# Optimization experiments

Hardware: AMD Instinct MI355X
Metric: run time of the kernel (lower is better)

## Reference

```python
import jax, jax.numpy as jnp
import numpy as np

N = 50000; E = 150000
NODE_IN = 16; EDGE_IN = 19; H = 32  # H = max(2*node_in, 32)
LEAK = 0.1; EPS = 1e-5
LAYER_DINS = (16, 32, 32)


def _leaky(x):
    return jnp.where(x >= 0, x, LEAK * x)


def _bn(x, g, b):
    # BatchNorm1d in training mode: batch statistics, biased variance
    m = x.mean(0)
    v = x.var(0)
    return (x - m) * jax.lax.rsqrt(v + EPS) * g + b


def setup_inputs() -> dict:
    key = jax.random.key(0)
    keys = iter(jax.random.split(key, 64))

    def rn(shape, s=0.05):
        return jax.random.normal(next(keys), shape, dtype=jnp.float32) * s

    inp = {
        'x': jax.random.normal(next(keys), (N, NODE_IN), dtype=jnp.float32),
        'edge_index': jax.random.randint(next(keys), (2, E), 0, N),
        'e': jax.random.normal(next(keys), (E, EDGE_IN), dtype=jnp.float32),
        'xbatch': jnp.zeros((N,), dtype=jnp.int32),
        'bn_node_g': jnp.ones((NODE_IN,), jnp.float32), 'bn_node_b': jnp.zeros((NODE_IN,), jnp.float32),
        'bn_edge_g': jnp.ones((EDGE_IN,), jnp.float32), 'bn_edge_b': jnp.zeros((EDGE_IN,), jnp.float32),
    }
    for l, din in enumerate(LAYER_DINS):
        inp[f'l{l}_nnW1'] = rn((EDGE_IN, din));      inp[f'l{l}_nnb1'] = jnp.zeros((din,), jnp.float32)
        inp[f'l{l}_nnW2'] = rn((din, din * H));       inp[f'l{l}_nnb2'] = jnp.zeros((din * H,), jnp.float32)
        inp[f'l{l}_root'] = rn((din, H));             inp[f'l{l}_bias'] = jnp.zeros((H,), jnp.float32)
    # MetaLayer predictor: EdgeModel(H, EDGE_IN, leak) and NodeModel(H, 2, leak)
    inp['em_W1'] = rn((2 * H + EDGE_IN, H)); inp['em_b1'] = jnp.zeros((H,), jnp.float32)
    inp['em_W2'] = rn((H, H));               inp['em_b2'] = jnp.zeros((H,), jnp.float32)
    inp['nm1_W1'] = rn((2 * H, H));          inp['nm1_b1'] = jnp.zeros((H,), jnp.float32)
    inp['nm1_W2'] = rn((H, H));              inp['nm1_b2'] = jnp.zeros((H,), jnp.float32)
    inp['nm2_W1'] = rn((2 * H, H));          inp['nm2_b1'] = jnp.zeros((H,), jnp.float32)
    inp['nm2_W2'] = rn((H, 2));              inp['nm2_b2'] = jnp.zeros((2,), jnp.float32)
    return inp


def _forward(x, e, edge_index, p):
    (bn_node_g, bn_node_b, bn_edge_g, bn_edge_b,
     l0_nnW1, l0_nnb1, l0_nnW2, l0_nnb2, l0_root, l0_bias,
     l1_nnW1, l1_nnb1, l1_nnW2, l1_nnb2, l1_root, l1_bias,
     l2_nnW1, l2_nnb1, l2_nnW2, l2_nnb2, l2_root, l2_bias,
     em_W1, em_b1, em_W2, em_b2,
     nm1_W1, nm1_b1, nm1_W2, nm1_b2,
     nm2_W1, nm2_b1, nm2_W2, nm2_b2) = p

    e = _bn(e, bn_edge_g, bn_edge_b)
    x = _bn(x, bn_node_g, bn_node_b)
    row, col = edge_index[0], edge_index[1]  # source, target (PyG convention)

    layers = [(l0_nnW1, l0_nnb1, l0_nnW2, l0_nnb2, l0_root, l0_bias),
              (l1_nnW1, l1_nnb1, l1_nnW2, l1_nnb2, l1_root, l1_bias),
              (l2_nnW1, l2_nnb1, l2_nnW2, l2_nnb2, l2_root, l2_bias)]
    for (W1, b1, W2, b2, root, bias), din in zip(layers, LAYER_DINS):
        # edge MLP -> per-edge weight matrix [E, din, H]
        w = _leaky(_leaky(e @ W1 + b1) @ W2 + b2).reshape(E, din, H)
        msg = jnp.einsum('ei,eio->eo', x[row], w)              # gather + per-edge matvec
        agg = jax.ops.segment_sum(msg, col, num_segments=N)     # scatter-add ('add' aggr)
        x = agg + x @ root + bias                                # NNConv root weight + bias

    # MetaLayer predictor
    e2 = _leaky(jnp.concatenate([x[row], x[col], e], axis=1) @ em_W1 + em_b1) @ em_W2 + em_b2
    h = _leaky(jnp.concatenate([x[row], e2], axis=1) @ nm1_W1 + nm1_b1) @ nm1_W2 + nm1_b2
    cnt = jnp.clip(jax.ops.segment_sum(jnp.ones((E,), x.dtype), col, num_segments=N), 1.0)
    agg = jax.ops.segment_sum(h, col, num_segments=N) / cnt[:, None]
    xo = _leaky(jnp.concatenate([x, agg], axis=1) @ nm2_W1 + nm2_b1) @ nm2_W2 + nm2_b2
    return jax.nn.log_softmax(xo, axis=1)  # [N, 2] node_pred


def reference(x, edge_index, e, xbatch,
              bn_node_g, bn_node_b, bn_edge_g, bn_edge_b,
              l0_nnW1, l0_nnb1, l0_nnW2, l0_nnb2, l0_root, l0_bias,
              l1_nnW1, l1_nnb1, l1_nnW2, l1_nnb2, l1_root, l1_bias,
              l2_nnW1, l2_nnb1, l2_nnW2, l2_nnb2, l2_root, l2_bias,
              em_W1, em_b1, em_W2, em_b2,
              nm1_W1, nm1_b1, nm1_W2, nm1_b2,
              nm2_W1, nm2_b1, nm2_W2, nm2_b2):
    p = (bn_node_g, bn_node_b, bn_edge_g, bn_edge_b,
         l0_nnW1, l0_nnb1, l0_nnW2, l0_nnb2, l0_root, l0_bias,
         l1_nnW1, l1_nnb1, l1_nnW2, l1_nnb2, l1_root, l1_bias,
         l2_nnW1, l2_nnb1, l2_nnW2, l2_nnb2, l2_root, l2_bias,
         em_W1, em_b1, em_W2, em_b2,
         nm1_W1, nm1_b1, nm1_W2, nm1_b2,
         nm2_W1, nm2_b1, nm2_W2, nm2_b2)
    return _forward(x, e, edge_index, p)
```

## Files before the change

### kernel.cpp

```cpp
#include <hip/hip_runtime.h>
#include <math.h>

constexpr int NN  = 50000;
constexpr int NE  = 150000;
constexpr int NIN = 16;
constexpr int EIN = 19;
constexpr int HD  = 32;
constexpr int NTILES = NE / 16;
constexpr int NBLK_E = 128;
constexpr int NBLK_X = 64;

#define LEAK  0.1f
#define BNEPS 1e-5f

typedef __attribute__((ext_vector_type(8))) short bfrag;
typedef __attribute__((ext_vector_type(4))) float f32x4;
typedef __attribute__((ext_vector_type(2))) float f32x2;
typedef __attribute__((ext_vector_type(4))) int   i32x4;

__device__ __forceinline__ float lky(float v){ return fmaxf(v, LEAK*v); }
__device__ __forceinline__ unsigned f2bf(float f){
  unsigned u = __float_as_uint(f);
  return ((u + 0x7FFFu + ((u >> 16) & 1u)) >> 16);
}
__device__ __forceinline__ void split8(const float* v, i32x4& h4, i32x4& l4){
  unsigned hs[8], ls[8];
  #pragma unroll
  for(int j = 0; j < 8; j++){
    unsigned hh = f2bf(v[j]);
    float hf = __uint_as_float(hh << 16);
    hs[j] = hh; ls[j] = f2bf(v[j] - hf);
  }
  h4[0] = (int)(hs[0] | (hs[1]<<16)); h4[1] = (int)(hs[2] | (hs[3]<<16));
  h4[2] = (int)(hs[4] | (hs[5]<<16)); h4[3] = (int)(hs[6] | (hs[7]<<16));
  l4[0] = (int)(ls[0] | (ls[1]<<16)); l4[1] = (int)(ls[2] | (ls[3]<<16));
  l4[2] = (int)(ls[4] | (ls[5]<<16)); l4[3] = (int)(ls[6] | (ls[7]<<16));
}

__global__ void zero_kernel(float* __restrict__ p, int n){
  int stride = gridDim.x * blockDim.x;
  for(int i = blockIdx.x*blockDim.x + threadIdx.x; i < n; i += stride) p[i] = 0.f;
}

__global__ __launch_bounds__(256) void stats_all_kernel(const float* __restrict__ e,
                                                        const float* __restrict__ x,
                                                        float* __restrict__ partial_e,
                                                        float* __restrict__ partial_x){
  __shared__ float red[4][40];
  const int tid = threadIdx.x, lane = tid & 63, wid = tid >> 6;
  if(blockIdx.x < NBLK_E){
    float s[EIN], q[EIN];
    #pragma unroll
    for(int c = 0; c < EIN; c++){ s[c] = 0.f; q[c] = 0.f; }
    const int gstride = NBLK_E * 256;
    for(int g = blockIdx.x*256 + tid; g < NE/4; g += gstride){
      const f32x4* p = (const f32x4*)(e + (size_t)g * 76);
      #pragma unroll
      for(int m = 0; m < 19; m++){
        f32x4 v = p[m];
        #pragma unroll
        for(int j = 0; j < 4; j++){
          int c = (4*m + j) % 19;
          s[c] += v[j]; q[c] = fmaf(v[j], v[j], q[c]);
        }
      }
    }
    #pragma unroll
    for(int off = 32; off; off >>= 1){
      #pragma unroll
      for(int c = 0; c < EIN; c++){ s[c] += __shfl_xor(s[c], off); q[c] += __shfl_xor(q[c], off); }
    }
    if(lane == 0){
      #pragma unroll
      for(int c = 0; c < EIN; c++){ red[wid][c] = s[c]; red[wid][20 + c] = q[c]; }
    }
    __syncthreads();
    if(tid < 39 && tid != 19)
      partial_e[blockIdx.x*40 + tid] = red[0][tid] + red[1][tid] + red[2][tid] + red[3][tid];
  } else {
    float s[NIN], q[NIN];
    #pragma unroll
    for(int c = 0; c < NIN; c++){ s[c] = 0.f; q[c] = 0.f; }
    const int bid = blockIdx.x - NBLK_E;
    const int gstride = NBLK_X * 256;
    for(int r = bid*256 + tid; r < NN; r += gstride){
      const f32x4* p = (const f32x4*)(x + (size_t)r * NIN);
      #pragma unroll
      for(int m = 0; m < 4; m++){
        f32x4 v = p[m];
        #pragma unroll
        for(int j = 0; j < 4; j++){
          int c = 4*m + j;
          s[c] += v[j]; q[c] = fmaf(v[j], v[j], q[c]);
        }
      }
    }
    #pragma unroll
    for(int off = 32; off; off >>= 1){
      #pragma unroll
      for(int c = 0; c < NIN; c++){ s[c] += __shfl_xor(s[c], off); q[c] += __shfl_xor(q[c], off); }
    }
    if(lane == 0){
      #pragma unroll
      for(int c = 0; c < NIN; c++){ red[wid][c] = s[c]; red[wid][16 + c] = q[c]; }
    }
    __syncthreads();
    if(tid < 32)
      partial_x[bid*32 + tid] = red[0][tid] + red[1][tid] + red[2][tid] + red[3][tid];
  }
}

__global__ __launch_bounds__(1024) void prep_kernel(const float* __restrict__ partial_e,
                                                    const float* __restrict__ partial_x,
                                                    const float* __restrict__ ge, const float* __restrict__ be,
                                                    const float* __restrict__ gx, const float* __restrict__ bx,
                                                    const float* __restrict__ l0W1, const float* __restrict__ l0b1,
                                                    const float* __restrict__ l1W1, const float* __restrict__ l1b1,
                                                    const float* __restrict__ l2W1, const float* __restrict__ l2b1,
                                                    const float* __restrict__ emW1, const float* __restrict__ emb1,
                                                    const float* __restrict__ emW2, const float* __restrict__ emb2,
                                                    const float* __restrict__ nm1W1, const float* __restrict__ nm1b1,
                                                    const float* __restrict__ nm1W2, const float* __restrict__ nm1b2,
                                                    float* __restrict__ ss_g, float* __restrict__ W1f,
                                                    float* __restrict__ b1f, float* __restrict__ biasP,
                                                    short* __restrict__ predpk){
  __shared__ float ss[70];
  __shared__ float emW1f[608];
  __shared__ float emb1f[32];
  __shared__ float predW[7168];
  const int t = threadIdx.x;

  if(t < EIN){
    float s = 0.f, q = 0.f;
    for(int b = 0; b < NBLK_E; b++){ s += partial_e[b*40 + t]; q += partial_e[b*40 + 20 + t]; }
    float m = s / (float)NE;
    float v = q / (float)NE - m*m;
    float sc = ge[t] * rsqrtf(v + BNEPS);
    ss[t] = sc; ss[EIN + t] = be[t] - m*sc;
  } else if(t >= 32 && t < 32 + NIN){
    int c = t - 32;
    float s = 0.f, q = 0.f;
    for(int b = 0; b < NBLK_X; b++){ s += partial_x[b*32 + c]; q += partial_x[b*32 + 16 + c]; }
    float m = s / (float)NN;
    float v = q / (float)NN - m*m;
    float sc = gx[c] * rsqrtf(v + BNEPS);
    ss[2*EIN + c] = sc; ss[2*EIN + NIN + c] = bx[c] - m*sc;
  }
  __syncthreads();
  if(t < 70) ss_g[t] = ss[t];

  if(t < 128){
    int seg = t >> 5, j = t & 31;
    if(seg == 0){
      if(j < NIN){
        float acc = l0b1[j];
        for(int k = 0; k < EIN; k++){
          W1f[0*640 + k*NIN + j] = ss[k] * l0W1[k*NIN + j];
          acc += ss[EIN+k] * l0W1[k*NIN + j];
        }
        b1f[0*32 + j] = acc;
      }
    } else if(seg == 1){
      float acc = l1b1[j];
      for(int k = 0; k < EIN; k++){
        W1f[1*640 + k*HD + j] = ss[k] * l1W1[k*HD + j];
        acc += ss[EIN+k] * l1W1[k*HD + j];
      }
      b1f[1*32 + j] = acc;
    } else if(seg == 2){
      float acc = l2b1[j];
      for(int k = 0; k < EIN; k++){
        W1f[2*640 + k*HD + j] = ss[k] * l2W1[k*HD + j];
        acc += ss[EIN+k] * l2W1[k*HD + j];
      }
      b1f[2*32 + j] = acc;
    } else {
      float acc = emb1[j];
      for(int k = 0; k < EIN; k++){
        emW1f[k*HD + j] = ss[k] * emW1[(2*HD+k)*HD + j];
        acc += ss[EIN+k] * emW1[(2*HD+k)*HD + j];
      }
      emb1f[j] = acc;
    }
  }
  __syncthreads();

  for(int i = t; i < 224*32; i += 1024){
    int k = i >> 5, n = i & 31;
    float v;
    if(k < 64)       v = emW1[k*32 + n];
    else if(k < 83)  v = emW1f[(k-64)*32 + n];
    else if(k < 96)  v = 0.f;
    else if(k < 128) v = emW2[(k-96)*32 + n];
    else if(k < 192) v = nm1W1[(k-128)*32 + n];
    else             v = nm1W2[(k-192)*32 + n];
    predW[i] = v;
  }
  if(t < 128){
    int s = t >> 5, n = t & 31;
    biasP[t] = (s==0) ? emb1f[n] : (s==1) ? emb2[n] : (s==2) ? nm1b1[n] : nm1b2[n];
  }
  __syncthreads();

  for(int idx = t; idx < 14*512; idx += 1024){
    int c = idx >> 9, l = (idx >> 3) & 63, j = idx & 7;
    int kbg = c >> 1, nc = c & 1;
    int k = kbg*32 + 8*(l>>4) + j;
    int n = nc*16 + (l & 15);
    predpk[idx] = (short)f2bf(predW[k*32 + n]);
  }
}

__global__ __launch_bounds__(256) void w2pack_all_kernel(const float* __restrict__ W20,
                                                         const float* __restrict__ W21,
                                                         const float* __restrict__ W22,
                                                         short* __restrict__ w2pk){
  int idx = blockIdx.x*256 + threadIdx.x;
  if(idx >= 81920) return;
  const float* W2; int DIN, base, ci;
  if(idx < 16384){ W2 = W20; DIN = 16; base = 0;     ci = idx; }
  else if(idx < 49152){ W2 = W21; DIN = 32; base = 32768; ci = idx - 16384; }
  else { W2 = W22; DIN = 32; base = 65536; ci = idx - 49152; }
  int c = ci >> 9, l = (ci >> 3) & 63, j = ci & 7;
  int k = 8*(l>>4) + j;
  int n = c*16 + (l & 15);
  float v = (k < DIN) ? W2[(size_t)k*(DIN*HD) + n] : 0.f;
  w2pk[base + ci] = (short)f2bf(v);
}

__global__ __launch_bounds__(256) void norm_root_kernel(const float* __restrict__ x,
                                                        const float* __restrict__ ssx,
                                                        const float* __restrict__ root,
                                                        const float* __restrict__ bias,
                                                        float* __restrict__ x_bn,
                                                        float* __restrict__ x_a){
  __shared__ float rs[NIN*HD];
  __shared__ float scs[NIN], shs[NIN], bs[HD];
  const int tid = threadIdx.x;
  for(int i = tid; i < NIN*HD; i += 256) rs[i] = root[i];
  if(tid < NIN){ scs[tid] = ssx[tid]; shs[tid] = ssx[NIN + tid]; }
  else if(tid < NIN + HD) bs[tid - NIN] = bias[tid - NIN];
  __syncthreads();

  int n = blockIdx.x*256 + tid;
  if(n >= NN) return;
  float xb[NIN];
  const f32x4* xp = (const f32x4*)(x + (size_t)n*NIN);
  #pragma unroll
  for(int g = 0; g < 4; g++){
    f32x4 v = xp[g];
    #pragma unroll
    for(int j = 0; j < 4; j++) xb[g*4+j] = fmaf(v[j], scs[g*4+j], shs[g*4+j]);
  }
  f32x4* obn = (f32x4*)(x_bn + (size_t)n*NIN);
  #pragma unroll
  for(int g = 0; g < 4; g++){
    f32x4 v; v[0]=xb[g*4]; v[1]=xb[g*4+1]; v[2]=xb[g*4+2]; v[3]=xb[g*4+3];
    obn[g] = v;
  }
  f32x4 a0 = *(const f32x4*)&bs[0],  a1 = *(const f32x4*)&bs[4];
  f32x4 a2 = *(const f32x4*)&bs[8],  a3 = *(const f32x4*)&bs[12];
  f32x4 a4 = *(const f32x4*)&bs[16], a5 = *(const f32x4*)&bs[20];
  f32x4 a6 = *(const f32x4*)&bs[24], a7 = *(const f32x4*)&bs[28];
  #pragma unroll
  for(int k = 0; k < NIN; k++){
    float v = xb[k];
    const f32x4* wp = (const f32x4*)&rs[k*HD];
    a0 = __builtin_elementwise_fma((f32x4){v,v,v,v}, wp[0], a0);
    a1 = __builtin_elementwise_fma((f32x4){v,v,v,v}, wp[1], a1);
    a2 = __builtin_elementwise_fma((f32x4){v,v,v,v}, wp[2], a2);
    a3 = __builtin_elementwise_fma((f32x4){v,v,v,v}, wp[3], a3);
    a4 = __builtin_elementwise_fma((f32x4){v,v,v,v}, wp[4], a4);
    a5 = __builtin_elementwise_fma((f32x4){v,v,v,v}, wp[5], a5);
    a6 = __builtin_elementwise_fma((f32x4){v,v,v,v}, wp[6], a6);
    a7 = __builtin_elementwise_fma((f32x4){v,v,v,v}, wp[7], a7);
  }
  f32x4* outp = (f32x4*)(x_a + (size_t)n*HD);
  outp[0]=a0; outp[1]=a1; outp[2]=a2; outp[3]=a3;
  outp[4]=a4; outp[5]=a5; outp[6]=a6; outp[7]=a7;
}

__global__ __launch_bounds__(256) void t1all_kernel(const float* __restrict__ eraw,
                                                    const float* __restrict__ W1f,
                                                    const float* __restrict__ b1f,
                                                    short* __restrict__ T10,
                                                    short* __restrict__ T11,
                                                    short* __restrict__ T12){
  int e = blockIdx.x*256 + threadIdx.x;
  if(e >= NE) return;
  const float* ep = eraw + (size_t)e*EIN;
  float eb[EIN];
  #pragma unroll
  for(int k = 0; k < EIN; k++) eb[k] = ep[k];

  {
    float tv[16];
    #pragma unroll
    for(int j = 0; j < 16; j++) tv[j] = b1f[j];
    #pragma unroll
    for(int k = 0; k < EIN; k++){
      float v = eb[k];
      #pragma unroll
      for(int j = 0; j < 16; j++) tv[j] = fmaf(v, W1f[k*16 + j], tv[j]);
    }
    unsigned pk[8];
    #pragma unroll
    for(int p = 0; p < 8; p++){
      float a = tv[2*p], b = tv[2*p+1];
      pk[p] = f2bf(fmaxf(a, LEAK*a)) | (f2bf(fmaxf(b, LEAK*b)) << 16);
    }
    i32x4* outp = (i32x4*)(T10 + (size_t)e*32);
    i32x4 v0; v0[0]=(int)pk[0]; v0[1]=(int)pk[1]; v0[2]=(int)pk[2]; v0[3]=(int)pk[3];
    i32x4 v1; v1[0]=(int)pk[4]; v1[1]=(int)pk[5]; v1[2]=(int)pk[6]; v1[3]=(int)pk[7];
    i32x4 zz; zz[0]=0; zz[1]=0; zz[2]=0; zz[3]=0;
    outp[0] = v0; outp[1] = v1; outp[2] = zz; outp[3] = zz;
  }
  #pragma unroll
  for(int l = 1; l < 3; l++){
    const float* Wl = W1f + l*640;
    const float* bl = b1f + l*32;
    short* Tl = (l == 1) ? T11 : T12;
    float tv[32];
    #pragma unroll
    for(int j = 0; j < 32; j++) tv[j] = bl[j];
    #pragma unroll
    for(int k = 0; k < EIN; k++){
      float v = eb[k];
      #pragma unroll
      for(int j = 0; j < 32; j++) tv[j] = fmaf(v, Wl[k*32 + j], tv[j]);
    }
    unsigned pk[16];
    #pragma unroll
    for(int p = 0; p < 16; p++){
      float a = tv[2*p], b = tv[2*p+1];
      pk[p] = f2bf(fmaxf(a, LEAK*a)) | (f2bf(fmaxf(b, LEAK*b)) << 16);
    }
    i32x4* outp = (i32x4*)(Tl + (size_t)e*32);
    #pragma unroll
    for(int g = 0; g < 4; g++){
      i32x4 v; v[0]=(int)pk[g*4]; v[1]=(int)pk[g*4+1]; v[2]=(int)pk[g*4+2]; v[3]=(int)pk[g*4+3];
      outp[g] = v;
    }
  }
}

template<int DIN>
__global__ __launch_bounds__(256) void rootv2_kernel(const float* __restrict__ xin,
                                                     const float* __restrict__ root,
                                                     const float* __restrict__ bias,
                                                     float* __restrict__ xout){
  int n = blockIdx.x*256 + threadIdx.x;
  if(n >= NN) return;
  float xr[DIN];
  const f32x4* xp = (const f32x4*)(xin + (size_t)n*DIN);
  #pragma unroll
  for(int g = 0; g < DIN/4; g++){ f32x4 v = xp[g];
    #pragma unroll
    for(int j = 0; j < 4; j++) xr[g*4+j] = v[j]; }
  float acc[HD];
  #pragma unroll
  for(int o = 0; o < HD; o++) acc[o] = bias[o];
  #pragma unroll
  for(int k = 0; k < DIN; k++){
    float v = xr[k];
    #pragma unroll
    for(int o = 0; o < HD; o++) acc[o] = fmaf(v, root[k*HD + o], acc[o]);
  }
  f32x4* outp = (f32x4*)(xout + (size_t)n*HD);
  #pragma unroll
  for(int g = 0; g < 8; g++){ f32x4 v; v[0]=acc[g*4]; v[1]=acc[g*4+1]; v[2]=acc[g*4+2]; v[3]=acc[g*4+3]; outp[g] = v; }
}

template<int DIN, int NCH, int HALVES>
__global__ __launch_bounds__(512) void msg6_kernel(const short* __restrict__ T1,
                                                   const int* __restrict__ rowp,
                                                   const int* __restrict__ colp,
                                                   const float* __restrict__ xin,
                                                   const short* __restrict__ w2p,
                                                   const float* __restrict__ b2,
                                                   float* __restrict__ xout){
  constexpr int CH = NCH / HALVES;
  __shared__ short w2s[CH*512];
  __shared__ float b2s[NCH*16];
  __shared__ float xgs[8][DIN][16];

  const int tid = threadIdx.x;
  const int l   = tid & 63;
  const int wid = tid >> 6;
  const int grp = l >> 4, lo16 = l & 15;
  const int tile = blockIdx.x*8 + wid;
  const bool active = tile < NTILES;
  const int e0 = tile * 16;

  if(active){
    int r = rowp[e0 + lo16];
    if(DIN == 32){
      const f32x4* xp = (const f32x4*)(xin + (size_t)r*32 + grp*8);
      f32x4 a = xp[0], b = xp[1];
      #pragma unroll
      for(int j = 0; j < 4; j++) xgs[wid][grp*8 + j][lo16]     = a[j];
      #pragma unroll
      for(int j = 0; j < 4; j++) xgs[wid][grp*8 + 4 + j][lo16] = b[j];
    } else {
      const f32x4* xp = (const f32x4*)(xin + (size_t)r*16 + grp*4);
      f32x4 a = xp[0];
      #pragma unroll
      for(int j = 0; j < 4; j++) xgs[wid][grp*4 + j][lo16] = a[j];
    }
  }

  bfrag af = {0,0,0,0,0,0,0,0};
  if(active) af = *(const bfrag*)(T1 + (size_t)(e0 + lo16)*32 + grp*8);

  f32x2 m0a = {0.f,0.f}, m0b = {0.f,0.f}, m1a = {0.f,0.f}, m1b = {0.f,0.f};

  for(int h = 0; h < HALVES; h++){
    if(h) __syncthreads();
    for(int t = tid; t < CH*64; t += 512)
      ((i32x4*)w2s)[t] = ((const i32x4*)w2p)[h*CH*64 + t];
    if(h == 0)
      for(int t = tid; t < NCH*16; t += 512) b2s[t] = b2[t];
    __syncthreads();

    if(active){
      #pragma unroll 4
      for(int i = 0; i < CH/2; i++){
        const int cg = h*CH + 2*i;
        const int ig = cg >> 1;
        float bv0 = b2s[cg*16 + lo16];
        float bv1 = b2s[(cg+1)*16 + lo16];
        f32x4 c0 = {bv0,bv0,bv0,bv0};
        f32x4 c1 = {bv1,bv1,bv1,bv1};
        bfrag b0 = *(const bfrag*)&w2s[((2*i  )*64 + l)*8];
        bfrag b1 = *(const bfrag*)&w2s[((2*i+1)*64 + l)*8];
        f32x4 u0 = __builtin_amdgcn_mfma_f32_16x16x32_bf16(af, b0, c0, 0, 0, 0);
        f32x4 u1 = __builtin_amdgcn_mfma_f32_16x16x32_bf16(af, b1, c1, 0, 0, 0);

        f32x4 xv = *(const f32x4*)&xgs[wid][ig][grp*4];
        f32x2 xva = {xv[0], xv[1]}, xvb = {xv[2], xv[3]};
        f32x2 u0a = {u0[0],u0[1]}, u0b = {u0[2],u0[3]};
        f32x2 u1a = {u1[0],u1[1]}, u1b = {u1[2],u1[3]};
        f32x2 a0a = __builtin_elementwise_max(u0a, u0a*LEAK);
        f32x2 a0b = __builtin_elementwise_max(u0b, u0b*LEAK);
        f32x2 a1a = __builtin_elementwise_max(u1a, u1a*LEAK);
        f32x2 a1b = __builtin_elementwise_max(u1b, u1b*LEAK);
        m0a = __builtin_elementwise_fma(xva, a0a, m0a);
        m0b = __builtin_elementwise_fma(xvb, a0b, m0b);
        m1a = __builtin_elementwise_fma(xva, a1a, m1a);
        m1b = __builtin_elementwise_fma(xvb, a1b, m1b);
      }
    }
  }

  if(active){
    float m0[4] = {m0a[0], m0a[1], m0b[0], m0b[1]};
    float m1[4] = {m1a[0], m1a[1], m1b[0], m1b[1]};
    #pragma unroll
    for(int reg = 0; reg < 4; reg++){
      int ce = colp[e0 + grp*4 + reg];
      atomicAdd(&xout[(size_t)ce*HD + lo16],      m0[reg]);
      atomicAdd(&xout[(size_t)ce*HD + 16 + lo16], m1[reg]);
    }
  }
}

__global__ __launch_bounds__(256, 4) void pred5_kernel(const float* __restrict__ x,
                                                       const float* __restrict__ eraw,
                                                       const int* __restrict__ rowp,
                                                       const int* __restrict__ colp,
                                                       const short* __restrict__ predpk,
                                                       const float* __restrict__ biasP,
                                                       float* __restrict__ agg,
                                                       float* __restrict__ cnt){
  __shared__ short fAhi[4][16][104];
  __shared__ short fAlo[4][16][104];
  __shared__ short uAhi[4][16][40];
  __shared__ short uAlo[4][16][40];

  const int tid = threadIdx.x;
  const int l = tid & 63, wid = tid >> 6;
  const int grp = l >> 4, lo16 = l & 15;

  bfrag wb[14];
  #pragma unroll
  for(int c = 0; c < 14; c++) wb[c] = *(const bfrag*)(predpk + ((size_t)c*64 + l)*8);
  float bP[8];
  #pragma unroll
  for(int s = 0; s < 4; s++){
    bP[s*2]   = biasP[s*32 + lo16];
    bP[s*2+1] = biasP[s*32 + 16 + lo16];
  }

  f32x4 z; z[0]=0.f; z[1]=0.f; z[2]=0.f; z[3]=0.f;
  const int tbase = (blockIdx.x*4 + wid) * 4;

  for(int tt = 0; tt < 4; tt++){
    const int tile = tbase + tt;
    if(tile >= NTILES) break;
    const int e0 = tile * 16;

    {
      float v[8];
      i32x4 h4, l4;
      int r = rowp[e0 + lo16];
      const float* xp = x + (size_t)r*32 + grp*8;
      #pragma unroll
      for(int j = 0; j < 8; j++) v[j] = xp[j];
      split8(v, h4, l4);
      *(i32x4*)&fAhi[wid][lo16][grp*8] = h4;
      *(i32x4*)&fAlo[wid][lo16][grp*8] = l4;

      int c = colp[e0 + lo16];
      const float* xq = x + (size_t)c*32 + grp*8;
      #pragma unroll
      for(int j = 0; j < 8; j++) v[j] = xq[j];
      split8(v, h4, l4);
      *(i32x4*)&fAhi[wid][lo16][32 + grp*8] = h4;
      *(i32x4*)&fAlo[wid][lo16][32 + grp*8] = l4;

      const float* ep = eraw + (size_t)(e0 + lo16)*EIN;
      #pragma unroll
      for(int j = 0; j < 8; j++){ int f = grp*8 + j; v[j] = (f < EIN) ? ep[f] : 0.f; }
      split8(v, h4, l4);
      *(i32x4*)&fAhi[wid][lo16][64 + grp*8] = h4;
      *(i32x4*)&fAlo[wid][lo16][64 + grp*8] = l4;
    }

    #pragma unroll
    for(int nc = 0; nc < 2; nc++){
      f32x4 acc = z;
      #pragma unroll
      for(int kb = 0; kb < 3; kb++){
        bfrag ah = *(const bfrag*)&fAhi[wid][lo16][kb*32 + grp*8];
        bfrag al = *(const bfrag*)&fAlo[wid][lo16][kb*32 + grp*8];
        acc = __builtin_amdgcn_mfma_f32_16x16x32_bf16(ah, wb[kb*2 + nc], acc, 0, 0, 0);
        acc = __builtin_amdgcn_mfma_f32_16x16x32_bf16(al, wb[kb*2 + nc], acc, 0, 0, 0);
      }
      int n = nc*16 + lo16;
      float bv = bP[nc];
      #pragma unroll
      for(int reg = 0; reg < 4; reg++){
        float uv = acc[reg] + bv; uv = fmaxf(uv, LEAK*uv);
        unsigned hh = f2bf(uv);
        float hf = __uint_as_float(hh << 16);
        uAhi[wid][grp*4 + reg][n] = (short)hh;
        uAlo[wid][grp*4 + reg][n] = (short)f2bf(uv - hf);
      }
    }

    #pragma unroll
    for(int nc = 0; nc < 2; nc++){
      f32x4 acc = z;
      bfrag ah = *(const bfrag*)&uAhi[wid][lo16][grp*8];
      bfrag al = *(const bfrag*)&uAlo[wid][lo16][grp*8];
      acc = __builtin_amdgcn_mfma_f32_16x16x32_bf16(ah, wb[6 + nc], acc, 0, 0, 0);
      acc = __builtin_amdgcn_mfma_f32_16x16x32_bf16(al, wb[6 + nc], acc, 0, 0, 0);
      int n = nc*16 + lo16;
      float bv = bP[2 + nc];
      #pragma unroll
      for(int reg = 0; reg < 4; reg++){
        float ev = acc[reg] + bv;
        unsigned hh = f2bf(ev);
        float hf = __uint_as_float(hh << 16);
        fAhi[wid][grp*4 + reg][32 + n] = (short)hh;
        fAlo[wid][grp*4 + reg][32 + n] = (short)f2bf(ev - hf);
      }
    }

    #pragma unroll
    for(int nc = 0; nc < 2; nc++){
      f32x4 acc = z;
      #pragma unroll
      for(int kb = 0; kb < 2; kb++){
        bfrag ah = *(const bfrag*)&fAhi[wid][lo16][kb*32 + grp*8];
        bfrag al = *(const bfrag*)&fAlo[wid][lo16][kb*32 + grp*8];
        acc = __builtin_amdgcn_mfma_f32_16x16x32_bf16(ah, wb[8 + kb*2 + nc], acc, 0, 0, 0);
        acc = __builtin_amdgcn_mfma_f32_16x16x32_bf16(al, wb[8 + kb*2 + nc], acc, 0, 0, 0);
      }
      int n = nc*16 + lo16;
      float bv = bP[4 + nc];
      #pragma unroll
      for(int reg = 0; reg < 4; reg++){
        float vv = acc[reg] + bv; vv = fmaxf(vv, LEAK*vv);
        unsigned hh = f2bf(vv);
        float hf = __uint_as_float(hh << 16);
        uAhi[wid][grp*4 + reg][n] = (short)hh;
        uAlo[wid][grp*4 + reg][n] = (short)f2bf(vv - hf);
      }
    }

    int ce[4];
    #pragma unroll
    for(int reg = 0; reg < 4; reg++) ce[reg] = colp[e0 + grp*4 + reg];

    #pragma unroll
    for(int nc = 0; nc < 2; nc++){
      f32x4 acc = z;
      bfrag ah = *(const bfrag*)&uAhi[wid][lo16][grp*8];
      bfrag al = *(const bfrag*)&uAlo[wid][lo16][grp*8];
      acc = __builtin_amdgcn_mfma_f32_16x16x32_bf16(ah, wb[12 + nc], acc, 0, 0, 0);
      acc = __builtin_amdgcn_mfma_f32_16x16x32_bf16(al, wb[12 + nc], acc, 0, 0, 0);
      int n = nc*16 + lo16;
      float bv = bP[6 + nc];
      #pragma unroll
      for(int reg = 0; reg < 4; reg++)
        atomicAdd(&agg[(size_t)ce[reg]*HD + n], acc[reg] + bv);
    }

    if(l < 16) atomicAdd(&cnt[colp[e0 + l]], 1.f);
  }
}

__global__ __launch_bounds__(256) void final2_kernel(const float* __restrict__ x,
                                                     const float* __restrict__ agg,
                                                     const float* __restrict__ cnt,
                                                     const float* __restrict__ W1,
                                                     const float* __restrict__ b1,
                                                     const float* __restrict__ W2,
                                                     const float* __restrict__ b2,
                                                     float* __restrict__ out){
  __shared__ float w1s[2*HD*HD];
  __shared__ float w2s[HD*2];
  __shared__ float b1s[HD];
  __shared__ float b2s[2];
  const int tid = threadIdx.x;
  for(int i = tid; i < 2*HD*HD; i += 256) w1s[i] = W1[i];
  if(tid < 64) w2s[tid] = W2[tid];
  if(tid < HD) b1s[tid] = b1[tid];
  if(tid < 2)  b2s[tid] = b2[tid];
  __syncthreads();

  int n = blockIdx.x*256 + tid;
  if(n >= NN) return;
  float inv = 1.f / fmaxf(cnt[n], 1.f);

  float xin[HD], ain[HD];
  const f32x4* xp = (const f32x4*)(x + (size_t)n*HD);
  const f32x4* ap = (const f32x4*)(agg + (size_t)n*HD);
  #pragma unroll
  for(int g = 0; g < 8; g++){
    f32x4 v = xp[g];
    #pragma unroll
    for(int j = 0; j < 4; j++) xin[g*4+j] = v[j];
  }
  #pragma unroll
  for(int g = 0; g < 8; g++){
    f32x4 v = ap[g];
    #pragma unroll
    for(int j = 0; j < 4; j++) ain[g*4+j] = v[j] * inv;
  }

  f32x4 a0 = *(const f32x4*)&b1s[0],  a1 = *(const f32x4*)&b1s[4];
  f32x4 a2 = *(const f32x4*)&b1s[8],  a3 = *(const f32x4*)&b1s[12];
  f32x4 a4 = *(const f32x4*)&b1s[16], a5 = *(const f32x4*)&b1s[20];
  f32x4 a6 = *(const f32x4*)&b1s[24], a7 = *(const f32x4*)&b1s[28];
  #pragma unroll
  for(int k = 0; k < HD; k++){
    float v = xin[k];
    const f32x4* wp = (const f32x4*)&w1s[k*HD];
    f32x4 vv = {v,v,v,v};
    a0 = __builtin_elementwise_fma(vv, wp[0], a0);
    a1 = __builtin_elementwise_fma(vv, wp[1], a1);
    a2 = __builtin_elementwise_fma(vv, wp[2], a2);
    a3 = __builtin_elementwise_fma(vv, wp[3], a3);
    a4 = __builtin_elementwise_fma(vv, wp[4], a4);
    a5 = __builtin_elementwise_fma(vv, wp[5], a5);
    a6 = __builtin_elementwise_fma(vv, wp[6], a6);
    a7 = __builtin_elementwise_fma(vv, wp[7], a7);
  }
  #pragma unroll
  for(int k = 0; k < HD; k++){
    float v = ain[k];
    const f32x4* wp = (const f32x4*)&w1s[(HD+k)*HD];
    f32x4 vv = {v,v,v,v};
    a0 = __builtin_elementwise_fma(vv, wp[0], a0);
    a1 = __builtin_elementwise_fma(vv, wp[1], a1);
    a2 = __builtin_elementwise_fma(vv, wp[2], a2);
    a3 = __builtin_elementwise_fma(vv, wp[3], a3);
    a4 = __builtin_elementwise_fma(vv, wp[4], a4);
    a5 = __builtin_elementwise_fma(vv, wp[5], a5);
    a6 = __builtin_elementwise_fma(vv, wp[6], a6);
    a7 = __builtin_elementwise_fma(vv, wp[7], a7);
  }

  float t[HD];
  *(f32x4*)&t[0]  = a0; *(f32x4*)&t[4]  = a1; *(f32x4*)&t[8]  = a2; *(f32x4*)&t[12] = a3;
  *(f32x4*)&t[16] = a4; *(f32x4*)&t[20] = a5; *(f32x4*)&t[24] = a6; *(f32x4*)&t[28] = a7;

  float o0 = b2s[0], o1 = b2s[1];
  #pragma unroll
  for(int k = 0; k < HD; k++){
    float v = lky(t[k]);
    o0 = fmaf(v, w2s[k*2],   o0);
    o1 = fmaf(v, w2s[k*2+1], o1);
  }

  float m  = fmaxf(o0, o1);
  float ls = m + logf(expf(o0 - m) + expf(o1 - m));
  out[(size_t)n*2]   = o0 - ls;
  out[(size_t)n*2+1] = o1 - ls;
}

extern "C" void kernel_launch(void* const* d_in, const int* in_sizes, int n_in,
                              void* d_out, int out_size, void* d_ws, size_t ws_size,
                              hipStream_t stream){
  const float* x  = (const float*)d_in[0];
  const int*   ei = (const int*)  d_in[1];
  const float* e  = (const float*)d_in[2];
  const float* bn_node_g = (const float*)d_in[4];
  const float* bn_node_b = (const float*)d_in[5];
  const float* bn_edge_g = (const float*)d_in[6];
  const float* bn_edge_b = (const float*)d_in[7];
  const float* lW1[3], *lb1[3], *lW2[3], *lb2[3], *lroot[3], *lbias[3];
  for(int l = 0; l < 3; l++){
    lW1[l]   = (const float*)d_in[8 + 6*l + 0];
    lb1[l]   = (const float*)d_in[8 + 6*l + 1];
    lW2[l]   = (const float*)d_in[8 + 6*l + 2];
    lb2[l]   = (const float*)d_in[8 + 6*l + 3];
    lroot[l] = (const float*)d_in[8 + 6*l + 4];
    lbias[l] = (const float*)d_in[8 + 6*l + 5];
  }
  const float* emW1  = (const float*)d_in[26];
  const float* emb1  = (const float*)d_in[27];
  const float* emW2  = (const float*)d_in[28];
  const float* emb2  = (const float*)d_in[29];
  const float* nm1W1 = (const float*)d_in[30];
  const float* nm1b1 = (const float*)d_in[31];
  const float* nm1W2 = (const float*)d_in[32];
  const float* nm1b2 = (const float*)d_in[33];
  const float* nm2W1 = (const float*)d_in[34];
  const float* nm2b1 = (const float*)d_in[35];
  const float* nm2W2 = (const float*)d_in[36];
  const float* nm2b2 = (const float*)d_in[37];

  const int* rowp = ei;
  const int* colp = ei + NE;

  float* ws   = (float*)d_ws;
  float* x_bn = ws;
  float* x_a  = x_bn + (size_t)NN*NIN;
  float* x_b  = x_a  + (size_t)NN*HD;
  float* scr  = x_b  + (size_t)NN*HD;
  float* partial_e = scr;
  float* partial_x = scr + 5120;
  float* ss_g      = scr + 7168;
  float* W1f       = scr + 7424;
  float* b1f       = scr + 9344;
  float* biasP     = scr + 9440;
  short* w2pk   = (short*)(scr + 16384);
  short* predpk = w2pk + 3*32768;
  short* T10    = predpk + 8192;
  short* T11    = T10 + (size_t)NE*32;
  short* T12    = T11 + (size_t)NE*32;
  float* agg    = (float*)T10;
  float* cnt    = agg + (size_t)NN*HD;

  stats_all_kernel<<<NBLK_E + NBLK_X, 256, 0, stream>>>(e, x, partial_e, partial_x);
  prep_kernel<<<1, 1024, 0, stream>>>(partial_e, partial_x,
                                      bn_edge_g, bn_edge_b, bn_node_g, bn_node_b,
                                      lW1[0], lb1[0], lW1[1], lb1[1], lW1[2], lb1[2],
                                      emW1, emb1, emW2, emb2,
                                      nm1W1, nm1b1, nm1W2, nm1b2,
                                      ss_g, W1f, b1f, biasP, predpk);
  w2pack_all_kernel<<<320, 256, 0, stream>>>(lW2[0], lW2[1], lW2[2], w2pk);
  t1all_kernel<<<(NE + 255)/256, 256, 0, stream>>>(e, W1f, b1f, T10, T11, T12);

  const int nblocks  = (NN + 255)/256;
  const int m6blocks = (NTILES + 7)/8;

  norm_root_kernel<<<nblocks, 256, 0, stream>>>(x, ss_g + 2*EIN, lroot[0], lbias[0], x_bn, x_a);
  msg6_kernel<NIN, 32, 2><<<m6blocks, 512, 0, stream>>>(T10, rowp, colp, x_bn,
                                                        w2pk + 0*32768, lb2[0], x_a);
  rootv2_kernel<HD><<<nblocks, 256, 0, stream>>>(x_a, lroot[1], lbias[1], x_b);
  msg6_kernel<HD, 64, 2><<<m6blocks, 512, 0, stream>>>(T11, rowp, colp, x_a,
                                                       w2pk + 1*32768, lb2[1], x_b);
  rootv2_kernel<HD><<<nblocks, 256, 0, stream>>>(x_b, lroot[2], lbias[2], x_a);
  msg6_kernel<HD, 64, 2><<<m6blocks, 512, 0, stream>>>(T12, rowp, colp, x_b,
                                                       w2pk + 2*32768, lb2[2], x_a);

  zero_kernel<<<2048, 256, 0, stream>>>(agg, NN*HD + NN);
  pred5_kernel<<<(NTILES + 15)/16, 256, 0, stream>>>(x_a, e, rowp, colp, predpk, biasP, agg, cnt);
  final2_kernel<<<(NN + 255)/256, 256, 0, stream>>>(x_a, agg, cnt,
                                                    nm2W1, nm2b1, nm2W2, nm2b2,
                                                    (float*)d_out);
}
```

Before: 219.9 us.

## Fuse node batchnorm into first message kernel, retune halves and pred tiling

Drops the separate x_bn buffer: the first message kernel now reads raw x and applies the batchnorm scale/shift on the fly, so the norm kernel only writes the root product. The HALVES template parameter for layers 1-2 goes from 2 to 4, and the prediction kernel handles 2 tiles per wave instead of 4, launching twice as many blocks. The custom zero kernel is replaced by hipMemsetAsync. This saves one N×16 write and read and adds parallelism, at the cost of redundant normalisation per edge gather.

```diff
diff --git a/kernel.cpp b/kernel.cpp
--- a/kernel.cpp
+++ b/kernel.cpp
@@ -35,11 +35,6 @@
   h4[2] = (int)(hs[4] | (hs[5]<<16)); h4[3] = (int)(hs[6] | (hs[7]<<16));
   l4[0] = (int)(ls[0] | (ls[1]<<16)); l4[1] = (int)(ls[2] | (ls[3]<<16));
   l4[2] = (int)(ls[4] | (ls[5]<<16)); l4[3] = (int)(ls[6] | (ls[7]<<16));
-}
-
-__global__ void zero_kernel(float* __restrict__ p, int n){
-  int stride = gridDim.x * blockDim.x;
-  for(int i = blockIdx.x*blockDim.x + threadIdx.x; i < n; i += stride) p[i] = 0.f;
 }
 
 __global__ __launch_bounds__(256) void stats_all_kernel(const float* __restrict__ e,
@@ -228,12 +223,11 @@
   w2pk[base + ci] = (short)f2bf(v);
 }
 
-__global__ __launch_bounds__(256) void norm_root_kernel(const float* __restrict__ x,
-                                                        const float* __restrict__ ssx,
-                                                        const float* __restrict__ root,
-                                                        const float* __restrict__ bias,
-                                                        float* __restrict__ x_bn,
-                                                        float* __restrict__ x_a){
+__global__ __launch_bounds__(256) void rootn_kernel(const float* __restrict__ x,
+                                                    const float* __restrict__ ssx,
+                                                    const float* __restrict__ root,
+                                                    const float* __restrict__ bias,
+                                                    float* __restrict__ x_a){
   __shared__ float rs[NIN*HD];
   __shared__ float scs[NIN], shs[NIN], bs[HD];
   const int tid = threadIdx.x;
@@ -252,12 +246,6 @@
     #pragma unroll
     for(int j = 0; j < 4; j++) xb[g*4+j] = fmaf(v[j], scs[g*4+j], shs[g*4+j]);
   }
-  f32x4* obn = (f32x4*)(x_bn + (size_t)n*NIN);
-  #pragma unroll
-  for(int g = 0; g < 4; g++){
-    f32x4 v; v[0]=xb[g*4]; v[1]=xb[g*4+1]; v[2]=xb[g*4+2]; v[3]=xb[g*4+3];
-    obn[g] = v;
-  }
   f32x4 a0 = *(const f32x4*)&bs[0],  a1 = *(const f32x4*)&bs[4];
   f32x4 a2 = *(const f32x4*)&bs[8],  a3 = *(const f32x4*)&bs[12];
   f32x4 a4 = *(const f32x4*)&bs[16], a5 = *(const f32x4*)&bs[20];
@@ -266,14 +254,15 @@
   for(int k = 0; k < NIN; k++){
     float v = xb[k];
     const f32x4* wp = (const f32x4*)&rs[k*HD];
-    a0 = __builtin_elementwise_fma((f32x4){v,v,v,v}, wp[0], a0);
-    a1 = __builtin_elementwise_fma((f32x4){v,v,v,v}, wp[1], a1);
-    a2 = __builtin_elementwise_fma((f32x4){v,v,v,v}, wp[2], a2);
-    a3 = __builtin_elementwise_fma((f32x4){v,v,v,v}, wp[3], a3);
-    a4 = __builtin_elementwise_fma((f32x4){v,v,v,v}, wp[4], a4);
-    a5 = __builtin_elementwise_fma((f32x4){v,v,v,v}, wp[5], a5);
-    a6 = __builtin_elementwise_fma((f32x4){v,v,v,v}, wp[6], a6);
-    a7 = __builtin_elementwise_fma((f32x4){v,v,v,v}, wp[7], a7);
+    f32x4 vv = {v,v,v,v};
+    a0 = __builtin_elementwise_fma(vv, wp[0], a0);
+    a1 = __builtin_elementwise_fma(vv, wp[1], a1);
+    a2 = __builtin_elementwise_fma(vv, wp[2], a2);
+    a3 = __builtin_elementwise_fma(vv, wp[3], a3);
+    a4 = __builtin_elementwise_fma(vv, wp[4], a4);
+    a5 = __builtin_elementwise_fma(vv, wp[5], a5);
+    a6 = __builtin_elementwise_fma(vv, wp[6], a6);
+    a7 = __builtin_elementwise_fma(vv, wp[7], a7);
   }
   f32x4* outp = (f32x4*)(x_a + (size_t)n*HD);
   outp[0]=a0; outp[1]=a1; outp[2]=a2; outp[3]=a3;
@@ -371,11 +360,12 @@
   for(int g = 0; g < 8; g++){ f32x4 v; v[0]=acc[g*4]; v[1]=acc[g*4+1]; v[2]=acc[g*4+2]; v[3]=acc[g*4+3]; outp[g] = v; }
 }
 
-template<int DIN, int NCH, int HALVES>
-__global__ __launch_bounds__(512) void msg6_kernel(const short* __restrict__ T1,
+template<int DIN, int NCH, int HALVES, int NORM>
+__global__ __launch_bounds__(512) void msg7_kernel(const short* __restrict__ T1,
                                                    const int* __restrict__ rowp,
                                                    const int* __restrict__ colp,
                                                    const float* __restrict__ xin,
+                                                   const float* __restrict__ ssx,
                                                    const short* __restrict__ w2p,
                                                    const float* __restrict__ b2,
                                                    float* __restrict__ xout){
@@ -404,6 +394,11 @@
     } else {
       const f32x4* xp = (const f32x4*)(xin + (size_t)r*16 + grp*4);
       f32x4 a = xp[0];
+      if(NORM){
+        f32x4 sc = *(const f32x4*)(ssx + grp*4);
+        f32x4 sh = *(const f32x4*)(ssx + NIN + grp*4);
+        a = __builtin_elementwise_fma(a, sc, sh);
+      }
       #pragma unroll
       for(int j = 0; j < 4; j++) xgs[wid][grp*4 + j][lo16] = a[j];
     }
@@ -464,7 +459,7 @@
   }
 }
 
-__global__ __launch_bounds__(256, 4) void pred5_kernel(const float* __restrict__ x,
+__global__ __launch_bounds__(256, 4) void pred6_kernel(const float* __restrict__ x,
                                                        const float* __restrict__ eraw,
                                                        const int* __restrict__ rowp,
                                                        const int* __restrict__ colp,
@@ -492,9 +487,9 @@
   }
 
   f32x4 z; z[0]=0.f; z[1]=0.f; z[2]=0.f; z[3]=0.f;
-  const int tbase = (blockIdx.x*4 + wid) * 4;
-
-  for(int tt = 0; tt < 4; tt++){
+  const int tbase = (blockIdx.x*4 + wid) * 2;
+
+  for(int tt = 0; tt < 2; tt++){
     const int tile = tbase + tt;
     if(tile >= NTILES) break;
     const int e0 = tile * 16;
@@ -737,10 +732,9 @@
   const int* colp = ei + NE;
 
   float* ws   = (float*)d_ws;
-  float* x_bn = ws;
-  float* x_a  = x_bn + (size_t)NN*NIN;
-  float* x_b  = x_a  + (size_t)NN*HD;
-  float* scr  = x_b  + (size_t)NN*HD;
+  float* x_a  = ws;
+  float* x_b  = x_a + (size_t)NN*HD;
+  float* scr  = x_b + (size_t)NN*HD;
   float* partial_e = scr;
   float* partial_x = scr + 5120;
   float* ss_g      = scr + 7168;
@@ -768,18 +762,21 @@
   const int nblocks  = (NN + 255)/256;
   const int m6blocks = (NTILES + 7)/8;
 
-  norm_root_kernel<<<nblocks, 256, 0, stream>>>(x, ss_g + 2*EIN, lroot[0], lbias[0], x_bn, x_a);
-  msg6_kernel<NIN, 32, 2><<<m6blocks, 512, 0, stream>>>(T10, rowp, colp, x_bn,
-                                                        w2pk + 0*32768, lb2[0], x_a);
+  rootn_kernel<<<nblocks, 256, 0, stream>>>(x, ss_g + 2*EIN, lroot[0], lbias[0], x_a);
+  msg7_kernel<NIN, 32, 2, 1><<<m6blocks, 512, 0, stream>>>(T10, rowp, colp, x,
+                                                           ss_g + 2*EIN,
+                                                           w2pk + 0*32768, lb2[0], x_a);
   rootv2_kernel<HD><<<nblocks, 256, 0, stream>>>(x_a, lroot[1], lbias[1], x_b);
-  msg6_kernel<HD, 64, 2><<<m6blocks, 512, 0, stream>>>(T11, rowp, colp, x_a,
-                                                       w2pk + 1*32768, lb2[1], x_b);
+  msg7_kernel<HD, 64, 4, 0><<<m6blocks, 512, 0, stream>>>(T11, rowp, colp, x_a,
+                                                          nullptr,
+                                                          w2pk + 1*32768, lb2[1], x_b);
   rootv2_kernel<HD><<<nblocks, 256, 0, stream>>>(x_b, lroot[2], lbias[2], x_a);
-  msg6_kernel<HD, 64, 2><<<m6blocks, 512, 0, stream>>>(T12, rowp, colp, x_b,
-                                                       w2pk + 2*32768, lb2[2], x_a);
-
-  zero_kernel<<<2048, 256, 0, stream>>>(agg, NN*HD + NN);
-  pred5_kernel<<<(NTILES + 15)/16, 256, 0, stream>>>(x_a, e, rowp, colp, predpk, biasP, agg, cnt);
+  msg7_kernel<HD, 64, 4, 0><<<m6blocks, 512, 0, stream>>>(T12, rowp, colp, x_b,
+                                                          nullptr,
+                                                          w2pk + 2*32768, lb2[2], x_a);
+
+  hipMemsetAsync(agg, 0, ((size_t)NN*HD + NN)*sizeof(float), stream);
+  pred6_kernel<<<(NTILES + 7)/8, 256, 0, stream>>>(x_a, e, rowp, colp, predpk, biasP, agg, cnt);
   final2_kernel<<<(NN + 255)/256, 256, 0, stream>>>(x_a, agg, cnt,
                                                     nm2W1, nm2b1, nm2W2, nm2b2,
                                                     (float*)d_out);
```

Result: slower. 228.6 us (+4.0%).
